# Optimization experiments

Hardware: AMD Instinct MI355X
Metric: run time of the kernel (lower is better)

Reference implementation:

```python
import jax, jax.numpy as jnp
import numpy as np
from jax import lax

EPS = 1e-5  # BatchNorm eps (inference mode)

def _bn(x, g, b, m, v):
    # inference batchnorm over channel axis 1 of NCHW
    s = g / jnp.sqrt(v + EPS)
    return x * s[None, :, None, None] + (b - m * s)[None, :, None, None]

def _conv1x1(w, x):
    # w: [O, C], x: [B, C, H, W]
    return jnp.einsum('oc,bchw->bohw', w, x)

def setup_inputs() -> dict:
    key = jax.random.key(0)
    ks = jax.random.split(key, 40)
    B, Cin, S = 8, 2048, 64
    R, D, H, NC = 128, 512, 64, 19
    f32 = jnp.float32
    def n(k, shape, scale):
        return jax.random.normal(k, shape, dtype=f32) * scale
    inp = {}
    inp['x'] = jax.random.normal(ks[0], (B, Cin, S, S), f32)
    inp['feat_w'] = n(ks[1], (D, Cin, 3, 3), 0.02)
    # 4 batchnorms: feat, encoding, fusion, conv6
    for i, name in enumerate(['bn1', 'bn2', 'bn3', 'bn4']):
        kk = jax.random.split(ks[2 + i], 4)
        inp[name + '_g'] = jax.random.uniform(kk[0], (D,), f32, 0.5, 1.5)
        inp[name + '_b'] = n(kk[1], (D,), 0.05)
        inp[name + '_m'] = n(kk[2], (D,), 0.1)
        inp[name + '_v'] = jax.random.uniform(kk[3], (D,), f32, 0.5, 1.5)
    inp['enc_w'] = n(ks[6], (D, D), 0.05)
    inp['fc_w'] = n(ks[7], (D, D), 0.05)
    inp['fc_b'] = n(ks[8], (D,), 0.05)
    inp['w1'] = n(ks[9], (R, D, D), 0.05)   # conv1_1[i]: 512->512 1x1
    inp['w2'] = n(ks[10], (R, H, H), 0.05)  # conv1_2[i]: 64->64 1x1
    inp['w3'] = n(ks[11], (R, H, H), 0.05)  # conv1_3[i]: 64->64 1x1
    inp['fusion_w'] = n(ks[12], (D, D), 0.05)
    inp['c6a_w'] = n(ks[13], (D, 2 * D), 0.05)
    inp['c6b_w'] = n(ks[14], (NC, D), 0.05)
    inp['c6b_b'] = n(ks[15], (NC,), 0.05)
    return inp

def reference(x, feat_w,
              bn1_g, bn1_b, bn1_m, bn1_v,
              bn2_g, bn2_b, bn2_m, bn2_v,
              bn3_g, bn3_b, bn3_m, bn3_v,
              bn4_g, bn4_b, bn4_m, bn4_v,
              enc_w, fc_w, fc_b, w1, w2, w3,
              fusion_w, c6a_w, c6b_w, c6b_b):
    # self.feat: 3x3 conv -> BN -> ReLU
    feat = jax.nn.relu(_bn(
        lax.conv_general_dilated(x, feat_w, (1, 1), 'SAME',
                                 dimension_numbers=('NCHW', 'OIHW', 'NCHW')),
        bn1_g, bn1_b, bn1_m, bn1_v))

    # EncModule (se_loss=False)
    enc = jax.nn.relu(_bn(_conv1x1(enc_w, feat), bn2_g, bn2_b, bn2_m, bn2_v))
    en = enc.mean(axis=(2, 3))                                # [B, 512]
    gamma = jax.nn.sigmoid(en @ fc_w.T + fc_b)                # [B, 512]
    se_out = jax.nn.relu(feat * (1.0 + gamma[:, :, None, None]))

    # ContextDecomp: pooled mode vectors (AdaptiveAvgPool2d(1) of permutes)
    Cvec = feat.mean(axis=(2, 3))   # [B, 512] channel vector
    Hvec = feat.mean(axis=(1, 2))   # [B, 64]  (avg over channel & height -> width axis)
    Wvec = feat.mean(axis=(1, 3))   # [B, 64]  (avg over channel & width  -> height axis)
    # all 128 rank-wise 1x1 convs + sigmoid, batched over rank r
    CC = jax.nn.sigmoid(jnp.einsum('roc,bc->bro', w1, Cvec))  # [B, R, 512]
    HH = jax.nn.sigmoid(jnp.einsum('roh,bh->bro', w2, Hvec))  # [B, R, 64]
    WW = jax.nn.sigmoid(jnp.einsum('row,bw->bro', w3, Wvec))  # [B, R, 64]
    # Tucker/CP reconstruction summed over ranks; torch layout puts the
    # width-derived vector (HH) on spatial axis 2 and height-derived (WW) on axis 3
    t1 = jnp.einsum('brc,bri,brj->bcij', CC, HH, WW) * 0.015625  # 1/64
    t = feat * (1.0 + t1)
    outs = jax.nn.relu(_bn(_conv1x1(fusion_w, t), bn3_g, bn3_b, bn3_m, bn3_v))

    # conv6 head: cat -> 1x1 conv -> BN -> ReLU -> (dropout eval=id) -> 1x1 conv
    cat = jnp.concatenate([outs, se_out], axis=1)              # [B, 1024, 64, 64]
    h6 = jax.nn.relu(_bn(_conv1x1(c6a_w, cat), bn4_g, bn4_b, bn4_m, bn4_v))
    out = _conv1x1(c6b_w, h6) + c6b_b[None, :, None, None]     # [B, 19, 64, 64]
    return out
```

## Files before the change

kernel.cpp:

```cpp
#include <hip/hip_runtime.h>
#include <stdint.h>
#include <stddef.h>

using u16 = unsigned short;
using u32 = unsigned int;
using u64 = unsigned long long;

typedef __attribute__((ext_vector_type(8))) short short8;
typedef __attribute__((ext_vector_type(4))) float f32x4;

#define DEV static __device__ __forceinline__

DEV float bf2f(u16 v){ union{u32 u; float f;} x; x.u = ((u32)v)<<16; return x.f; }
DEV u16 f2bf(float f){ union{float f; u32 u;} x; x.f = f; u32 r = (x.u + 0x7FFFu + ((x.u>>16)&1u))>>16; return (u16)r; }
DEV float lo16(u32 u){ union{u32 u; float f;} x; x.u = u<<16; return x.f; }
DEV float hi16(u32 u){ union{u32 u; float f;} x; x.u = u & 0xFFFF0000u; return x.f; }

DEV void gload16(const u16* g, u16* l){
  __builtin_amdgcn_global_load_lds((const __attribute__((address_space(1))) void*)g,
                                   (__attribute__((address_space(3))) void*)l, 16, 0, 0);
}

#define BAR    __builtin_amdgcn_s_barrier()
#define SCHED0 __builtin_amdgcn_sched_barrier(0)
#define PRIO1  __builtin_amdgcn_s_setprio(1)
#define PRIO0  __builtin_amdgcn_s_setprio(0)
#define VMC4   asm volatile("s_waitcnt vmcnt(4)" ::: "memory")
#define VMC0   asm volatile("s_waitcnt vmcnt(0)" ::: "memory")

__global__ __launch_bounds__(512, 2)
void conv_gemm256(const u16* __restrict__ xp, const u16* __restrict__ wt,
                  u16* __restrict__ O, const float* __restrict__ sb,
                  float* __restrict__ Cvec, float* __restrict__ Hvec,
                  float* __restrict__ Wvec)
{
  constexpr int NT = 288;
  __shared__ u16 smA[2*256*64];
  __shared__ u16 smB[2*256*64];
  const int t = threadIdx.x;
  const int lane = t & 63;
  const int wv = t >> 6;
  const int wr = wv >> 2, wc = wv & 3;
  const int mt = blockIdx.x, nt = blockIdx.y, b = blockIdx.z;
  const int ij0 = mt*256, n0 = nt*256;
  const u16* Ab = xp + (size_t)b*66*66*2048;

  const int tA   = t >> 3;
  const int sc8  = ((t&7) ^ ((t>>3)&7)) * 8;
  const int ldsc = (t&7) * 8;
  const int qB   = t >> 8;
  const int rB   = (t>>3) & 31;

  f32x4 acc[8][4];
  #pragma unroll
  for (int i=0;i<8;++i)
    #pragma unroll
    for (int j=0;j<4;++j) acc[i][j] = (f32x4){0.f,0.f,0.f,0.f};

  short8 aR[4][2];
  short8 bR[2][2][2];

#define STG_A(dst, s, kt_) do{ \
    const int ktc = (kt_) < NT ? (kt_) : (NT-1); \
    const int tap = ktc>>5; const int ty = (tap*11)>>5; const int tx = tap - ty*3; \
    const size_t ko = ((size_t)(ktc&31))<<6; \
    _Pragma("unroll") for (int l=0;l<2;++l){ \
      const int row = (s)*64 + tA + l*128; \
      const u16* src = Ab + ((size_t)((mt*4 + (s) + l*2 + ty)*66 + tA + tx))*2048 + ko + sc8; \
      gload16(src, (dst) + row*64 + ldsc); } }while(0)

#define STG_B(dst, s, kt_) do{ \
    const int ktc = (kt_) < NT ? (kt_) : (NT-1); \
    const int tap = ktc>>5; \
    const size_t ko = (size_t)tap*2048 + (((size_t)(ktc&31))<<6); \
    _Pragma("unroll") for (int l=0;l<2;++l){ \
      const int row = (l*2 + qB)*64 + (s)*32 + rB; \
      const u16* src = wt + ((size_t)(n0 + row))*9*2048 + ko + sc8; \
      gload16(src, (dst) + row*64 + ldsc); } }while(0)

#define LDA_(base, mh) do{ _Pragma("unroll") for(int mi=0;mi<4;++mi){ \
    const int r = wr*128 + (mh)*64 + mi*16 + (lane&15); \
    _Pragma("unroll") for(int kk=0;kk<2;++kk){ \
      const int ch = (kk*4 + (lane>>4)) ^ (r&7); \
      aR[mi][kk] = *(const short8*)&(base)[r*64 + ch*8]; } } }while(0)
#define LDB_(base, nh) do{ _Pragma("unroll") for(int ni=0;ni<2;++ni){ \
    const int r = wc*64 + (nh)*32 + ni*16 + (lane&15); \
    _Pragma("unroll") for(int kk=0;kk<2;++kk){ \
      const int ch = (kk*4 + (lane>>4)) ^ (r&7); \
      bR[nh][ni][kk] = *(const short8*)&(base)[r*64 + ch*8]; } } }while(0)
#define MFMAQ(mh, nh) do{ _Pragma("unroll") for(int mi=0;mi<4;++mi) \
    _Pragma("unroll") for(int ni=0;ni<2;++ni){ \
      acc[(mh)*4+mi][(nh)*2+ni] = __builtin_amdgcn_mfma_f32_16x16x32_bf16(aR[mi][0], bR[nh][ni][0], acc[(mh)*4+mi][(nh)*2+ni],0,0,0); \
      acc[(mh)*4+mi][(nh)*2+ni] = __builtin_amdgcn_mfma_f32_16x16x32_bf16(aR[mi][1], bR[nh][ni][1], acc[(mh)*4+mi][(nh)*2+ni],0,0,0); } }while(0)

  STG_A(smA, 0, 0);
  STG_B(smB, 0, 0);
  STG_B(smB, 1, 0);
  STG_A(smA, 1, 0);
  VMC4;
  BAR; SCHED0;

  for (int j=0; j<NT; ++j) {
    const int p = j & 1;
    const u16* As = smA + (p<<14);
    const u16* Bs = smB + (p<<14);
    u16* Aalt = smA + ((p^1)<<14);
    u16* Balt = smB + ((p^1)<<14);

    LDA_(As, 0); LDB_(Bs, 0);
    STG_A(Aalt, 0, j+1);
    BAR; SCHED0;
    PRIO1; MFMAQ(0,0); PRIO0;
    VMC4;
    BAR; SCHED0;

    LDB_(Bs, 1);
    STG_B(Balt, 0, j+1);
    BAR; SCHED0;
    PRIO1; MFMAQ(0,1); PRIO0;
    VMC4;
    BAR; SCHED0;

    LDA_(As, 1);
    STG_B(Balt, 1, j+1);
    BAR; SCHED0;
    PRIO1; MFMAQ(1,0); PRIO0;
    BAR; SCHED0;

    STG_A(Aalt, 1, j+1);
    BAR; SCHED0;
    PRIO1; MFMAQ(1,1); PRIO0;
    VMC4;
    BAR; SCHED0;
  }

  VMC0;
  BAR;
  float* red = (float*)smA;
  if (t < 324) red[t] = 0.f;
  BAR;

  float xs[4][4];
  #pragma unroll
  for (int q=0;q<4;++q)
    #pragma unroll
    for (int j2=0;j2<4;++j2) xs[q][j2] = 0.f;
  float ys0 = 0.f, ys1 = 0.f;

  #pragma unroll
  for (int n=0; n<4; ++n) {
    const int cloc = wc*64 + (n>>1)*32 + (n&1)*16 + (lane&15);
    const int col = n0 + cloc;
    const float s = sb[col], bb = sb[512+col];
    float cs = 0.f;
    #pragma unroll
    for (int a=0; a<8; ++a) {
      const int row0 = ij0 + wr*128 + (a>>2)*64 + (a&3)*16 + ((lane>>4)<<2);
      #pragma unroll
      for (int j2=0; j2<4; ++j2) {
        const size_t idx = ((size_t)(b*4096 + row0 + j2))*512 + col;
        float v = acc[a][n][j2]*s + bb;
        v = v > 0.f ? v : 0.f;
        O[idx] = f2bf(v);
        cs += v;
        xs[a&3][j2] += v;
        if (a < 4) ys0 += v; else ys1 += v;
      }
    }
    atomicAdd(&red[cloc], cs);
  }
  #pragma unroll
  for (int off=1; off<16; off<<=1)
    #pragma unroll
    for (int q=0;q<4;++q)
      #pragma unroll
      for (int j2=0;j2<4;++j2) xs[q][j2] += __shfl_xor(xs[q][j2], off);
  if ((lane & 15) == 0) {
    #pragma unroll
    for (int q=0;q<4;++q)
      #pragma unroll
      for (int j2=0;j2<4;++j2)
        atomicAdd(&red[256 + q*16 + (lane>>4)*4 + j2], xs[q][j2]);
  }
  #pragma unroll
  for (int off=1; off<64; off<<=1) { ys0 += __shfl_xor(ys0, off); ys1 += __shfl_xor(ys1, off); }
  if (lane == 0) {
    atomicAdd(&red[320 + wr*2 + 0], ys0);
    atomicAdd(&red[320 + wr*2 + 1], ys1);
  }
  BAR;
  if (t < 256)       atomicAdd(&Cvec[b*512 + n0 + t], red[t]*(1.0f/4096.0f));
  else if (t < 320)  atomicAdd(&Hvec[b*64 + (t-256)], red[t]*(1.0f/32768.0f));
  else if (t < 324)  atomicAdd(&Wvec[b*64 + (ij0>>6) + (t-320)], red[t]*(1.0f/32768.0f));
#undef STG_A
#undef STG_B
#undef LDA_
#undef LDB_
#undef MFMAQ
}

template<int V>
__global__ __launch_bounds__(512, 2)
void gemm256(const u16* __restrict__ A0, const u16* __restrict__ A1,
             const u16* __restrict__ Bw0, const u16* __restrict__ Bw1,
             u16* __restrict__ O, const float* __restrict__ sb,
             float* __restrict__ en)
{
  constexpr int NTALL = (V==4) ? 16 : 8;
  __shared__ u16 smA[2*256*64];
  __shared__ u16 smB[2*256*64];
  const int t = threadIdx.x;
  const int lane = t & 63;
  const int wv = t >> 6;
  const int wr = wv >> 2, wc = wv & 3;
  const int mt = blockIdx.x, nt = blockIdx.y, b = blockIdx.z;
  const int ij0 = mt*256, n0 = nt*256;
  const u16* A0b = A0 + (size_t)b*4096*512;
  const u16* A1b = (V==4) ? (A1 + (size_t)b*4096*512) : nullptr;
  const u16* B1b = (V==4) ? (Bw1 + (size_t)b*512*512) : nullptr;

  const int tA   = t >> 3;
  const int sc8  = ((t&7) ^ ((t>>3)&7)) * 8;
  const int ldsc = (t&7) * 8;
  const int qB   = t >> 8;
  const int rB   = (t>>3) & 31;

  f32x4 acc[8][4];
  #pragma unroll
  for (int i=0;i<8;++i)
    #pragma unroll
    for (int j=0;j<4;++j) acc[i][j] = (f32x4){0.f,0.f,0.f,0.f};

  short8 aR[4][2];
  short8 bR[2][2][2];

#define STG_A(dst, s, kt_) do{ \
    const int ktc = (kt_) < NTALL ? (kt_) : (NTALL-1); \
    const u16* Abase = (V==4 && ktc>=8) ? A1b : A0b; \
    const size_t ko = ((size_t)(ktc&7))<<6; \
    _Pragma("unroll") for (int l=0;l<2;++l){ \
      const int row = (s)*64 + tA + l*128; \
      const u16* src = Abase + (size_t)(ij0 + row)*512 + ko + sc8; \
      gload16(src, (dst) + row*64 + ldsc); } }while(0)

#define STG_B(dst, s, kt_) do{ \
    const int ktc = (kt_) < NTALL ? (kt_) : (NTALL-1); \
    const u16* Bbase = (V==4 && ktc>=8) ? B1b : Bw0; \
    const size_t ko = ((size_t)(ktc&7))<<6; \
    _Pragma("unroll") for (int l=0;l<2;++l){ \
      const int row = (l*2 + qB)*64 + (s)*32 + rB; \
      const u16* src = Bbase + (size_t)(n0 + row)*512 + ko + sc8; \
      gload16(src, (dst) + row*64 + ldsc); } }while(0)

#define LDA_(base, mh) do{ _Pragma("unroll") for(int mi=0;mi<4;++mi){ \
    const int r = wr*128 + (mh)*64 + mi*16 + (lane&15); \
    _Pragma("unroll") for(int kk=0;kk<2;++kk){ \
      const int ch = (kk*4 + (lane>>4)) ^ (r&7); \
      aR[mi][kk] = *(const short8*)&(base)[r*64 + ch*8]; } } }while(0)
#define LDB_(base, nh) do{ _Pragma("unroll") for(int ni=0;ni<2;++ni){ \
    const int r = wc*64 + (nh)*32 + ni*16 + (lane&15); \
    _Pragma("unroll") for(int kk=0;kk<2;++kk){ \
      const int ch = (kk*4 + (lane>>4)) ^ (r&7); \
      bR[nh][ni][kk] = *(const short8*)&(base)[r*64 + ch*8]; } } }while(0)
#define MFMAQ(mh, nh) do{ _Pragma("unroll") for(int mi=0;mi<4;++mi) \
    _Pragma("unroll") for(int ni=0;ni<2;++ni){ \
      acc[(mh)*4+mi][(nh)*2+ni] = __builtin_amdgcn_mfma_f32_16x16x32_bf16(aR[mi][0], bR[nh][ni][0], acc[(mh)*4+mi][(nh)*2+ni],0,0,0); \
      acc[(mh)*4+mi][(nh)*2+ni] = __builtin_amdgcn_mfma_f32_16x16x32_bf16(aR[mi][1], bR[nh][ni][1], acc[(mh)*4+mi][(nh)*2+ni],0,0,0); } }while(0)

  STG_A(smA, 0, 0);
  STG_B(smB, 0, 0);
  STG_B(smB, 1, 0);
  STG_A(smA, 1, 0);
  VMC4;
  BAR; SCHED0;

  for (int j=0; j<NTALL; ++j) {
    const int p = j & 1;
    const u16* As = smA + (p<<14);
    const u16* Bs = smB + (p<<14);
    u16* Aalt = smA + ((p^1)<<14);
    u16* Balt = smB + ((p^1)<<14);

    LDA_(As, 0); LDB_(Bs, 0);
    STG_A(Aalt, 0, j+1);
    BAR; SCHED0;
    PRIO1; MFMAQ(0,0); PRIO0;
    VMC4;
    BAR; SCHED0;

    LDB_(Bs, 1);
    STG_B(Balt, 0, j+1);
    BAR; SCHED0;
    PRIO1; MFMAQ(0,1); PRIO0;
    VMC4;
    BAR; SCHED0;

    LDA_(As, 1);
    STG_B(Balt, 1, j+1);
    BAR; SCHED0;
    PRIO1; MFMAQ(1,0); PRIO0;
    BAR; SCHED0;

    STG_A(Aalt, 1, j+1);
    BAR; SCHED0;
    PRIO1; MFMAQ(1,1); PRIO0;
    VMC4;
    BAR; SCHED0;
  }
  VMC0;

  if constexpr (V==1) {
    #pragma unroll
    for (int n=0; n<4; ++n) {
      const int col = n0 + wc*64 + (n>>1)*32 + (n&1)*16 + (lane&15);
      const float s = sb[col], bb = sb[512+col];
      float cs = 0.f;
      #pragma unroll
      for (int a=0; a<8; ++a) {
        #pragma unroll
        for (int j2=0; j2<4; ++j2) {
          float v = acc[a][n][j2]*s + bb;
          cs += (v > 0.f) ? v : 0.f;
        }
      }
      cs += __shfl_xor(cs, 16);
      cs += __shfl_xor(cs, 32);
      if (lane < 16) atomicAdd(&en[b*512 + col], cs * (1.0f/4096.0f));
    }
  } else {
    #pragma unroll
    for (int n=0; n<4; ++n) {
      const int col = n0 + wc*64 + (n>>1)*32 + (n&1)*16 + (lane&15);
      const float s = sb[col], bb = sb[512+col];
      #pragma unroll
      for (int a=0; a<8; ++a) {
        const int row0 = ij0 + wr*128 + (a>>2)*64 + (a&3)*16 + ((lane>>4)<<2);
        #pragma unroll
        for (int j2=0; j2<4; ++j2) {
          const size_t idx = ((size_t)(b*4096 + row0 + j2))*512 + col;
          float v = acc[a][n][j2]*s + bb;
          O[idx] = f2bf(v > 0.f ? v : 0.f);
        }
      }
    }
  }
#undef STG_A
#undef STG_B
#undef LDA_
#undef LDB_
#undef MFMAQ
}

template<int V>
__global__ __launch_bounds__(256)
void gemm128(const u16* __restrict__ A, const u16* __restrict__ Bw, u16* __restrict__ O,
             const u16* __restrict__ feat, const u16* __restrict__ B2,
             const float* __restrict__ sb, float* __restrict__ en)
{
  constexpr int KSEG = 128;
  __shared__ u16 smA[128*64];
  __shared__ u16 smB[128*64];
  const int tid = threadIdx.x;
  const int lane = tid & 63;
  const int wv = tid >> 6;
  const int wr = wv >> 1, wc = wv & 1;
  const int mt = blockIdx.x, nt = blockIdx.y, b = blockIdx.z;
  const int ij0 = mt*128, n0 = nt*128;
  const int srow = tid >> 3, schunk = tid & 7;

  f32x4 acc[4][4];
  #pragma unroll
  for (int i=0;i<4;++i)
    #pragma unroll
    for (int j=0;j<4;++j) acc[i][j] = (f32x4){0.f,0.f,0.f,0.f};

  const u16* Ab = A + (size_t)b*4096*128;
  const u16* Bb = Bw + (size_t)b*512*128;

  for (int kt=0; kt<KSEG/64; ++kt) {
    const int k0 = kt*64;
    #pragma unroll
    for (int i=0;i<4;++i) {
      const int row = i*32 + srow;
      const int sc = schunk ^ (row & 7);
      gload16(Ab + (size_t)(ij0+row)*128 + (k0 + sc*8), &smA[row*64 + schunk*8]);
    }
    #pragma unroll
    for (int i=0;i<4;++i) {
      const int row = i*32 + srow;
      const int sc = schunk ^ (row & 7);
      gload16(Bb + (size_t)(n0+row)*128 + (k0 + sc*8), &smB[row*64 + schunk*8]);
    }
    __syncthreads();
    #pragma unroll
    for (int ks=0; ks<2; ++ks) {
      short8 av[4], bv[4];
      #pragma unroll
      for (int mi=0;mi<4;++mi) {
        const int r = wr*64 + mi*16 + (lane & 15);
        const int ch = (ks*4 + (lane>>4)) ^ (r & 7);
        av[mi] = *(const short8*)&smA[r*64 + ch*8];
      }
      #pragma unroll
      for (int ni=0;ni<4;++ni) {
        const int r = wc*64 + ni*16 + (lane & 15);
        const int ch = (ks*4 + (lane>>4)) ^ (r & 7);
        bv[ni] = *(const short8*)&smB[r*64 + ch*8];
      }
      #pragma unroll
      for (int mi=0;mi<4;++mi)
        #pragma unroll
        for (int ni=0;ni<4;++ni)
          acc[mi][ni] = __builtin_amdgcn_mfma_f32_16x16x32_bf16(av[mi], bv[ni], acc[mi][ni], 0, 0, 0);
    }
    __syncthreads();
  }

  #pragma unroll
  for (int ni=0;ni<4;++ni) {
    const int col = n0 + wc*64 + ni*16 + (lane & 15);
    #pragma unroll
    for (int mi=0;mi<4;++mi) {
      const int row0 = ij0 + wr*64 + mi*16 + ((lane>>4)<<2);
      #pragma unroll
      for (int j=0;j<4;++j) {
        const size_t idx = ((size_t)(b*4096 + row0 + j))*512 + col;
        O[idx] = f2bf(bf2f(feat[idx]) * (1.0f + acc[mi][ni][j]));
      }
    }
  }
}

__global__ __launch_bounds__(256)
void prep_weights(const float* __restrict__ fw, const float* __restrict__ encw,
                  const float* __restrict__ fusw, const float* __restrict__ c6aw,
                  const float* g1,const float* b1,const float* m1,const float* v1,
                  const float* g2,const float* b2,const float* m2,const float* v2,
                  const float* g3,const float* b3,const float* m3,const float* v3,
                  const float* g4,const float* b4,const float* m4,const float* v4,
                  u16* __restrict__ wt, u16* __restrict__ encb,
                  u16* __restrict__ fusb, u16* __restrict__ c6a1,
                  float* __restrict__ bnsb)
{
  const int bx = blockIdx.x, t = threadIdx.x;
  if (bx < 512) {
    __shared__ float slab[2048*9];
    const int o = bx;
    const float4* src4 = (const float4*)(fw + (size_t)o*2048*9);
    float4* slab4 = (float4*)slab;
    #pragma unroll
    for (int i=0; i<18; ++i) slab4[i*256 + t] = src4[i*256 + t];
    __syncthreads();
    #pragma unroll
    for (int tt=0; tt<9; ++tt) {
      #pragma unroll
      for (int i=0; i<8; ++i) {
        const int c = i*256 + t;
        wt[((size_t)o*9 + tt)*2048 + c] = f2bf(slab[c*9 + tt]);
      }
    }
  } else if (bx < 1536) {
    const int i = (bx-512)*256 + t;
    encb[i] = f2bf(encw[i]);
  } else if (bx < 2560) {
    const int i = (bx-1536)*256 + t;
    fusb[i] = f2bf(fusw[i]);
  } else if (bx < 3584) {
    const int i = (bx-2560)*256 + t;
    c6a1[i] = f2bf(c6aw[(size_t)(i>>9)*1024 + (i&511)]);
  } else {
    const int c = (bx-3584)*256 + t;
    if (c < 512) {
      const float eps = 1e-5f;
      float s1 = g1[c]*rsqrtf(v1[c]+eps); bnsb[c]      = s1; bnsb[512+c]  = b1[c]-m1[c]*s1;
      float s2 = g2[c]*rsqrtf(v2[c]+eps); bnsb[1024+c] = s2; bnsb[1536+c] = b2[c]-m2[c]*s2;
      float s3 = g3[c]*rsqrtf(v3[c]+eps); bnsb[2048+c] = s3; bnsb[2560+c] = b3[c]-m3[c]*s3;
      float s4 = g4[c]*rsqrtf(v4[c]+eps); bnsb[3072+c] = s4; bnsb[3584+c] = b4[c]-m4[c]*s4;
    }
  }
}

__global__ __launch_bounds__(256)
void pad_x(const float* __restrict__ x, u16* __restrict__ xp)
{
  __shared__ u16 tile[256*68];
  const int bx = blockIdx.x;
  const int cb = bx & 7, y = (bx>>3) & 63, b = bx >> 9;
  const int t = threadIdx.x;
  const int xg = t & 15, crow = t >> 4;
  for (int it=0; it<16; ++it) {
    const int cl = it*16 + crow;
    const float4 v = *(const float4*)&x[(((size_t)b*2048 + cb*256 + cl)*64 + y)*64 + xg*4];
    const u64 pk = (u64)f2bf(v.x) | ((u64)f2bf(v.y)<<16) | ((u64)f2bf(v.z)<<32) | ((u64)f2bf(v.w)<<48);
    *(u64*)&tile[cl*68 + xg*4] = pk;
  }
  __syncthreads();
  const size_t rowbase = (size_t)(b*66 + y + 1)*66;
  for (int px=0; px<64; ++px)
    xp[(rowbase + px + 1)*2048 + cb*256 + t] = tile[t*68 + px];
  xp[rowbase*2048 + cb*256 + t] = 0;
  xp[(rowbase + 65)*2048 + cb*256 + t] = 0;
  if (y == 0) {
    const size_t rb = (size_t)(b*66)*66;
    for (int px=0; px<66; ++px) xp[(rb+px)*2048 + cb*256 + t] = 0;
  }
  if (y == 63) {
    const size_t rb = (size_t)(b*66 + 65)*66;
    for (int px=0; px<66; ++px) xp[(rb+px)*2048 + cb*256 + t] = 0;
  }
}

__global__ __launch_bounds__(256)
void small1(const float* __restrict__ en, const float* __restrict__ fcw, const float* __restrict__ fcb,
            const float* __restrict__ w1, const float* __restrict__ Cvec,
            const float* __restrict__ w2, const float* __restrict__ w3,
            const float* __restrict__ Hvec, const float* __restrict__ Wvec,
            float* __restrict__ gamma, u16* __restrict__ CCT,
            float* __restrict__ HH, float* __restrict__ WW)
{
  const int bx = blockIdx.x, t = threadIdx.x;
  if (bx < 8) {
    __shared__ float enl[512];
    const int b = bx;
    for (int c=t;c<512;c+=256) enl[c] = en[b*512+c];
    __syncthreads();
    for (int o=t;o<512;o+=256) {
      float a = fcb[o];
      const float* wr = fcw + (size_t)o*512;
      for (int c=0;c<512;++c) a += enl[c]*wr[c];
      gamma[b*512+o] = 1.0f/(1.0f+__expf(-a));
    }
  } else if (bx < 136) {
    __shared__ float hl[512], wl[512];
    const int r = bx - 8;
    for (int i=t;i<512;i+=256){ hl[i]=Hvec[i]; wl[i]=Wvec[i]; }
    __syncthreads();
    const int i = t & 63, bh = t >> 6;
    for (int bb=bh; bb<8; bb+=4) {
      float sh=0.f, sw=0.f;
      const float* w2r = w2 + ((size_t)r*64 + i)*64;
      const float* w3r = w3 + ((size_t)r*64 + i)*64;
      #pragma unroll 8
      for (int h=0;h<64;++h){ sh += w2r[h]*hl[bb*64+h]; sw += w3r[h]*wl[bb*64+h]; }
      HH[((size_t)bb*128 + r)*64 + i] = 1.0f/(1.0f+__expf(-sh));
      WW[((size_t)bb*128 + r)*64 + i] = 1.0f/(1.0f+__expf(-sw));
    }
  } else {
    __shared__ float cv[4096];
    for (int i=t;i<4096;i+=256) cv[i] = Cvec[i];
    __syncthreads();
    const int rr    = (bx-136) >> 2;
    const int obase = ((bx-136) & 3) * 128;
    const int lane = t & 63, wg = t >> 6;
    const float* w1r = w1 + (size_t)rr*512*512;
    for (int i=0; i<32; ++i) {
      const int o = obase + wg*32 + i;
      const float* row = w1r + (size_t)o*512;
      const float4 wA = *(const float4*)(row + lane*8);
      const float4 wB = *(const float4*)(row + lane*8 + 4);
      float ab[8];
      #pragma unroll
      for (int bb=0;bb<8;++bb) {
        const float4 cA = *(const float4*)&cv[bb*512 + lane*8];
        const float4 cB = *(const float4*)&cv[bb*512 + lane*8 + 4];
        ab[bb] = wA.x*cA.x + wA.y*cA.y + wA.z*cA.z + wA.w*cA.w
               + wB.x*cB.x + wB.y*cB.y + wB.z*cB.z + wB.w*cB.w;
      }
      #pragma unroll
      for (int off=32; off; off>>=1)
        #pragma unroll
        for (int bb=0;bb<8;++bb) ab[bb] += __shfl_xor(ab[bb], off);
      #pragma unroll
      for (int bb=0;bb<8;++bb)
        if (lane == bb)
          CCT[((size_t)bb*512 + o)*128 + rr] = f2bf((1.0f/(1.0f+__expf(-ab[bb]))) * 0.015625f);
    }
  }
}

__global__ __launch_bounds__(256)
void small2(const float* __restrict__ c6aw, const float* __restrict__ gamma,
            const float* __restrict__ HH, const float* __restrict__ WW,
            u16* __restrict__ w2b, u16* __restrict__ HWT)
{
  const int bx = blockIdx.x, t = threadIdx.x;
  if (bx < 4096) {
    const int b = bx >> 9, o = bx & 511;
    const float* src = c6aw + (size_t)o*1024 + 512;
    const float* gmv = gamma + b*512;
    u16* dst = w2b + ((size_t)b*512 + o)*512;
    for (int c=t;c<512;c+=256) dst[c] = f2bf(src[c]*(1.0f+gmv[c]));
  } else {
    __shared__ float wwl[64*129];
    __shared__ float hhy[128];
    const int idx = bx - 4096;
    const int b = idx >> 6, y = idx & 63;
    for (int g=t; g<8192; g+=256){ const int r=g>>6, xx=g&63; wwl[xx*129+r] = WW[((size_t)b*128+r)*64+xx]; }
    if (t < 128) hhy[t] = HH[((size_t)b*128 + t)*64 + y];
    __syncthreads();
    const int r2 = (t & 63)*2, xg = t >> 6;
    for (int xx=xg; xx<64; xx+=4) {
      const float v0 = hhy[r2]   * wwl[xx*129 + r2];
      const float v1 = hhy[r2+1] * wwl[xx*129 + r2 + 1];
      const u32 pk = (u32)f2bf(v0) | ((u32)f2bf(v1)<<16);
      *(u32*)&HWT[((size_t)(b*4096 + y*64 + xx))*128 + r2] = pk;
    }
  }
}

__global__ __launch_bounds__(256)
void c6b_head(const u16* __restrict__ h6, const float* __restrict__ w,
              const float* __restrict__ bias, float* __restrict__ out)
{
  __shared__ float part[128*21];
  const int t = threadIdx.x;
  const int pl = t & 127, half = t >> 7;
  const int pix = (blockIdx.x << 7) + pl;
  const int b = pix >> 12, ij = pix & 4095;
  float acc[19];
  #pragma unroll
  for (int o=0;o<19;++o) acc[o] = 0.f;
  const u16* hp = h6 + (size_t)pix*512 + half*256;
  const float* wh = w + half*256;
  for (int c0=0;c0<256;c0+=8) {
    const uint4 d = *(const uint4*)(hp + c0);
    const float f0=lo16(d.x),f1=hi16(d.x),f2=lo16(d.y),f3=hi16(d.y),
                f4=lo16(d.z),f5=hi16(d.z),f6=lo16(d.w),f7=hi16(d.w);
    #pragma unroll
    for (int o=0;o<19;++o) {
      const float* wr = wh + o*512 + c0;
      acc[o] += f0*wr[0] + f1*wr[1] + f2*wr[2] + f3*wr[3]
              + f4*wr[4] + f5*wr[5] + f6*wr[6] + f7*wr[7];
    }
  }
  if (half) {
    #pragma unroll
    for (int o=0;o<19;++o) part[pl*21 + o] = acc[o];
  }
  __syncthreads();
  if (!half) {
    #pragma unroll
    for (int o=0;o<19;++o)
      out[((size_t)(b*19 + o))*4096 + ij] = acc[o] + part[pl*21 + o] + bias[o];
  }
}

extern "C" void kernel_launch(void* const* d_in, const int* in_sizes, int n_in,
                              void* d_out, int out_size, void* d_ws, size_t ws_size,
                              hipStream_t stream)
{
  (void)in_sizes; (void)n_in; (void)out_size;
  const float* x     = (const float*)d_in[0];
  const float* fw    = (const float*)d_in[1];
  const float* bnp[16];
  for (int i=0;i<16;++i) bnp[i] = (const float*)d_in[2+i];
  const float* enc_w = (const float*)d_in[18];
  const float* fc_w  = (const float*)d_in[19];
  const float* fc_b  = (const float*)d_in[20];
  const float* w1    = (const float*)d_in[21];
  const float* w2    = (const float*)d_in[22];
  const float* w3    = (const float*)d_in[23];
  const float* fus_w = (const float*)d_in[24];
  const float* c6a_w = (const float*)d_in[25];
  const float* c6b_w = (const float*)d_in[26];
  const float* c6b_b = (const float*)d_in[27];

  char* ws = (char*)d_ws;
  constexpr size_t OFF_XP=0, OFF_T=0, OFF_OUTS=33554432ull, OFF_H6=67108864ull,
    OFF_WT=142737408ull, OFF_FEAT=161611776ull, OFF_HWT=195166208ull, OFF_W2B=203554816ull,
    OFF_CCT=207749120ull, OFF_ENCB=208797696ull, OFF_FUSB=209321984ull, OFF_C6A1=209846272ull,
    OFF_HH=210370560ull, OFF_WW=210632704ull, OFF_EN=210894848ull, OFF_CV=210911232ull,
    OFF_HV=210927616ull, OFF_WV=210929664ull, OFF_GAMMA=210931712ull, OFF_BNSB=210948096ull,
    NEEDED=210964480ull;
  if (ws_size < NEEDED) return;

  u16* xp    = (u16*)(ws + OFF_XP);
  u16* tb    = (u16*)(ws + OFF_T);
  u16* outs  = (u16*)(ws + OFF_OUTS);
  u16* h6    = (u16*)(ws + OFF_H6);
  u16* wt    = (u16*)(ws + OFF_WT);
  u16* featb = (u16*)(ws + OFF_FEAT);
  u16* hwt   = (u16*)(ws + OFF_HWT);
  u16* w2b   = (u16*)(ws + OFF_W2B);
  u16* cct   = (u16*)(ws + OFF_CCT);
  u16* encb  = (u16*)(ws + OFF_ENCB);
  u16* fusb  = (u16*)(ws + OFF_FUSB);
  u16* c6a1  = (u16*)(ws + OFF_C6A1);
  float* HH  = (float*)(ws + OFF_HH);
  float* WW  = (float*)(ws + OFF_WW);
  float* en  = (float*)(ws + OFF_EN);
  float* Cv  = (float*)(ws + OFF_CV);
  float* Hv  = (float*)(ws + OFF_HV);
  float* Wv  = (float*)(ws + OFF_WV);
  float* gm  = (float*)(ws + OFF_GAMMA);
  float* bnsb= (float*)(ws + OFF_BNSB);

  hipMemsetAsync(ws + OFF_EN, 0, 36864, stream);

  prep_weights<<<3586,256,0,stream>>>(fw, enc_w, fus_w, c6a_w,
      bnp[0],bnp[1],bnp[2],bnp[3], bnp[4],bnp[5],bnp[6],bnp[7],
      bnp[8],bnp[9],bnp[10],bnp[11], bnp[12],bnp[13],bnp[14],bnp[15],
      wt, encb, fusb, c6a1, bnsb);
  pad_x<<<4096,256,0,stream>>>(x, xp);
  conv_gemm256<<<dim3(16,2,8),512,0,stream>>>(xp, wt, featb, bnsb, Cv, Hv, Wv);
  gemm256<1><<<dim3(16,2,8),512,0,stream>>>(featb, nullptr, encb, nullptr, nullptr, bnsb+1024, en);
  small1<<<648,256,0,stream>>>(en, fc_w, fc_b, w1, Cv, w2, w3, Hv, Wv, gm, cct, HH, WW);
  small2<<<4608,256,0,stream>>>(c6a_w, gm, HH, WW, w2b, hwt);
  gemm128<2><<<dim3(32,4,8),256,0,stream>>>(hwt, cct, tb, featb, nullptr, nullptr, nullptr);
  gemm256<3><<<dim3(16,2,8),512,0,stream>>>(tb, nullptr, fusb, nullptr, outs, bnsb+2048, nullptr);
  gemm256<4><<<dim3(16,2,8),512,0,stream>>>(outs, featb, c6a1, w2b, h6, bnsb+3072, nullptr);
  c6b_head<<<256,256,0,stream>>>(h6, c6b_w, c6b_b, (float*)d_out);
}
```

Baseline: 887.3 us.

## Simplify conv GEMM main loop to single-barrier prefetch-all then compute

Replaces the four-phase interleaved loop, which staged loads, LDS fragment reads and MFMA quarters separated by barriers, with a loop that issues all next-tile global-to-LDS copies up front. It then reads all A/B fragments into two A register sets, runs all MFMAs, and waits on vmcnt(0) plus one barrier. The aim is to cut barrier and scheduling overhead per k-step. In exchange it doubles A fragment registers and loses the fine-grained overlap between memory waits and compute.

Result: slower. 974.9 us (+9.9%).

```diff
diff --git a/kernel.cpp b/kernel.cpp
--- a/kernel.cpp
+++ b/kernel.cpp
@@ -57,7 +57,8 @@
     #pragma unroll
     for (int j=0;j<4;++j) acc[i][j] = (f32x4){0.f,0.f,0.f,0.f};
 
-  short8 aR[4][2];
+  short8 aR0[4][2];
+  short8 aR1[4][2];
   short8 bR[2][2][2];
 
 #define STG_A(dst, s, kt_) do{ \
@@ -78,27 +79,27 @@
       const u16* src = wt + ((size_t)(n0 + row))*9*2048 + ko + sc8; \
       gload16(src, (dst) + row*64 + ldsc); } }while(0)
 
-#define LDA_(base, mh) do{ _Pragma("unroll") for(int mi=0;mi<4;++mi){ \
+#define LDA_(arr, base, mh) do{ _Pragma("unroll") for(int mi=0;mi<4;++mi){ \
     const int r = wr*128 + (mh)*64 + mi*16 + (lane&15); \
     _Pragma("unroll") for(int kk=0;kk<2;++kk){ \
       const int ch = (kk*4 + (lane>>4)) ^ (r&7); \
-      aR[mi][kk] = *(const short8*)&(base)[r*64 + ch*8]; } } }while(0)
+      arr[mi][kk] = *(const short8*)&(base)[r*64 + ch*8]; } } }while(0)
 #define LDB_(base, nh) do{ _Pragma("unroll") for(int ni=0;ni<2;++ni){ \
     const int r = wc*64 + (nh)*32 + ni*16 + (lane&15); \
     _Pragma("unroll") for(int kk=0;kk<2;++kk){ \
       const int ch = (kk*4 + (lane>>4)) ^ (r&7); \
       bR[nh][ni][kk] = *(const short8*)&(base)[r*64 + ch*8]; } } }while(0)
-#define MFMAQ(mh, nh) do{ _Pragma("unroll") for(int mi=0;mi<4;++mi) \
+#define MFMAQ(arr, mh, nh) do{ _Pragma("unroll") for(int mi=0;mi<4;++mi) \
     _Pragma("unroll") for(int ni=0;ni<2;++ni){ \
-      acc[(mh)*4+mi][(nh)*2+ni] = __builtin_amdgcn_mfma_f32_16x16x32_bf16(aR[mi][0], bR[nh][ni][0], acc[(mh)*4+mi][(nh)*2+ni],0,0,0); \
-      acc[(mh)*4+mi][(nh)*2+ni] = __builtin_amdgcn_mfma_f32_16x16x32_bf16(aR[mi][1], bR[nh][ni][1], acc[(mh)*4+mi][(nh)*2+ni],0,0,0); } }while(0)
+      acc[(mh)*4+mi][(nh)*2+ni] = __builtin_amdgcn_mfma_f32_16x16x32_bf16(arr[mi][0], bR[nh][ni][0], acc[(mh)*4+mi][(nh)*2+ni],0,0,0); \
+      acc[(mh)*4+mi][(nh)*2+ni] = __builtin_amdgcn_mfma_f32_16x16x32_bf16(arr[mi][1], bR[nh][ni][1], acc[(mh)*4+mi][(nh)*2+ni],0,0,0); } }while(0)
 
   STG_A(smA, 0, 0);
   STG_B(smB, 0, 0);
   STG_B(smB, 1, 0);
   STG_A(smA, 1, 0);
-  VMC4;
-  BAR; SCHED0;
+  VMC0;
+  BAR;
 
   for (int j=0; j<NT; ++j) {
     const int p = j & 1;
@@ -107,34 +108,27 @@
     u16* Aalt = smA + ((p^1)<<14);
     u16* Balt = smB + ((p^1)<<14);
 
-    LDA_(As, 0); LDB_(Bs, 0);
     STG_A(Aalt, 0, j+1);
-    BAR; SCHED0;
-    PRIO1; MFMAQ(0,0); PRIO0;
-    VMC4;
-    BAR; SCHED0;
-
+    STG_B(Balt, 0, j+1);
+    STG_B(Balt, 1, j+1);
+    STG_A(Aalt, 1, j+1);
+
+    LDA_(aR0, As, 0);
+    LDB_(Bs, 0);
     LDB_(Bs, 1);
-    STG_B(Balt, 0, j+1);
-    BAR; SCHED0;
-    PRIO1; MFMAQ(0,1); PRIO0;
-    VMC4;
-    BAR; SCHED0;
-
-    LDA_(As, 1);
-    STG_B(Balt, 1, j+1);
-    BAR; SCHED0;
-    PRIO1; MFMAQ(1,0); PRIO0;
-    BAR; SCHED0;
-
-    STG_A(Aalt, 1, j+1);
-    BAR; SCHED0;
-    PRIO1; MFMAQ(1,1); PRIO0;
-    VMC4;
-    BAR; SCHED0;
-  }
-
-  VMC0;
+    LDA_(aR1, As, 1);
+
+    PRIO1;
+    MFMAQ(aR0, 0, 0);
+    MFMAQ(aR0, 0, 1);
+    MFMAQ(aR1, 1, 0);
+    MFMAQ(aR1, 1, 1);
+    PRIO0;
+
+    VMC0;
+    BAR;
+  }
+
   BAR;
   float* red = (float*)smA;
   if (t < 324) red[t] = 0.f;
```
